# Optimization experiments

Measured on AMD Instinct MI355X. Metric: run time of the kernel, lower is better.

The kernel has to match this reference:

```python
import jax, jax.numpy as jnp
import numpy as np

B, T, C, H = 8, 2048, 1024, 128  # batch, seq, n_embed, head_size


def setup_inputs() -> dict:
    key = jax.random.key(0)
    ks = jax.random.split(key, 7)
    s = 1.0 / np.sqrt(C)
    return {
        "x": jax.random.normal(ks[0], (B, T, C), dtype=jnp.float32),
        "Wq": jax.random.uniform(ks[1], (C, H), jnp.float32, -s, s),
        "bq": jax.random.uniform(ks[2], (H,), jnp.float32, -s, s),
        "Wk": jax.random.uniform(ks[3], (C, H), jnp.float32, -s, s),
        "bk": jax.random.uniform(ks[4], (H,), jnp.float32, -s, s),
        "Wv": jax.random.uniform(ks[5], (C, H), jnp.float32, -s, s),
        "bv": jax.random.uniform(ks[6], (H,), jnp.float32, -s, s),
    }


def reference(x, Wq, bq, Wk, bk, Wv, bv):
    # Projections: [B, T, H]
    Q = jnp.einsum("btc,ch->bth", x, Wq) + bq
    K = jnp.einsum("btc,ch->bth", x, Wk) + bk
    V = jnp.einsum("btc,ch->bth", x, Wv) + bv
    # Scores scaled by n_embed**-0.5 (faithful to source, which uses C not head_size)
    scale = jnp.asarray(C, x.dtype) ** -0.5
    scores = jnp.einsum("bqh,bkh->bqk", Q, K) * scale  # [B, T, T]
    causal = jnp.tril(jnp.ones((T, T), dtype=bool))
    scores = jnp.where(causal, scores, jnp.asarray(-jnp.inf, x.dtype))
    attn = jax.nn.softmax(scores, axis=-1)
    # dropout p=0.0 (eval) -> identity
    return jnp.einsum("bqk,bkh->bqh", attn, V)
```

## Files before the change

kernel.cpp:

```cpp
#include <hip/hip_runtime.h>
#include <hip/hip_bf16.h>
#include <math.h>

typedef __attribute__((ext_vector_type(4))) float f32x4;
typedef __attribute__((ext_vector_type(8))) short s16x8;
typedef __attribute__((ext_vector_type(4))) short s16x4;

#define NB 8
#define NT 2048
#define NC 1024
#define NH 128
#define QSCALE 0.04508422002778f

__device__ __forceinline__ short f2bf(float f) {
  union { float f; unsigned u; } v; v.f = f;
  unsigned r = v.u + 0x7fffu + ((v.u >> 16) & 1u);
  return (short)(r >> 16);
}

__device__ __forceinline__ void glds16(const short* g, short* l) {
  __builtin_amdgcn_global_load_lds(
      (const __attribute__((address_space(1))) unsigned int*)g,
      (__attribute__((address_space(3))) unsigned int*)l, 16, 0, 0);
}

__global__ __launch_bounds__(256)
void wt_kernel(const float* __restrict__ Wq, const float* __restrict__ Wk,
               const float* __restrict__ Wv, short* __restrict__ Wt) {
  __shared__ short T[64 * 72];
  const int tid = threadIdx.x;
  const int k0 = blockIdx.x * 64, n0 = blockIdx.y * 64, proj = blockIdx.z;
  const float* W = (proj == 0) ? Wq : ((proj == 1) ? Wk : Wv);
#pragma unroll
  for (int u = 0; u < 4; u++) {
    int row = u * 16 + (tid >> 4);
    int col4 = (tid & 15) * 4;
    float4 v = *(const float4*)(W + (size_t)(k0 + row) * NH + n0 + col4);
    T[(col4 + 0) * 72 + row] = f2bf(v.x);
    T[(col4 + 1) * 72 + row] = f2bf(v.y);
    T[(col4 + 2) * 72 + row] = f2bf(v.z);
    T[(col4 + 3) * 72 + row] = f2bf(v.w);
  }
  __syncthreads();
#pragma unroll
  for (int u = 0; u < 2; u++) {
    int c = tid + 256 * u;
    int n = c >> 3, c8 = c & 7;
    s16x8 v = *(const s16x8*)(T + n * 72 + c8 * 8);
    *(s16x8*)(Wt + (size_t)proj * (NH * NC) + (size_t)(n0 + n) * NC + k0 + c8 * 8) = v;
  }
}

__global__ __launch_bounds__(256, 3)
void proj_kernel(const float* __restrict__ x, const short* __restrict__ Wt,
                 const float* __restrict__ bq, const float* __restrict__ bk,
                 const float* __restrict__ bv,
                 short* __restrict__ Qb, short* __restrict__ Kb, short* __restrict__ Vtb) {
  __shared__ __align__(16) short smem[2 * 12288];

  const int tid = threadIdx.x;
  const int w = tid >> 6, lane = tid & 63;
  const int lr = lane & 15, lg = lane >> 4;

  const int bid = blockIdx.x;
  const int orig = (bid & 7) * 96 + (bid >> 3);
  const int proj = orig >> 8;
  const int m0 = (orig & 255) * 64;

  const short* Wtp = Wt + (size_t)proj * (NH * NC);

  f32x4 acc[8];
#pragma unroll
  for (int i = 0; i < 8; i++) acc[i] = {0.f, 0.f, 0.f, 0.f};

  const int s0 = 2 * tid, s1 = 2 * tid + 1;
  const int ar0 = s0 >> 3, ac0 = s0 & 7, ar1 = s1 >> 3, ac1 = s1 & 7;
  const float* asrc0base = x + (size_t)(m0 + ar0) * NC + ((ac0 ^ (ar0 & 7)) * 8);
  const float* asrc1base = x + (size_t)(m0 + ar1) * NC + ((ac1 ^ (ar1 & 7)) * 8);

  float4 a00, a01, a10, a11;

  auto stageA_load = [&](int k0) {
    a00 = *(const float4*)(asrc0base + k0);
    a01 = *(const float4*)(asrc0base + k0 + 4);
    a10 = *(const float4*)(asrc1base + k0);
    a11 = *(const float4*)(asrc1base + k0 + 4);
  };
  auto stageA_write = [&](int buf) {
    s16x8 v;
    v[0] = f2bf(a00.x); v[1] = f2bf(a00.y); v[2] = f2bf(a00.z); v[3] = f2bf(a00.w);
    v[4] = f2bf(a01.x); v[5] = f2bf(a01.y); v[6] = f2bf(a01.z); v[7] = f2bf(a01.w);
    *(s16x8*)(smem + buf * 12288 + s0 * 8) = v;
    v[0] = f2bf(a10.x); v[1] = f2bf(a10.y); v[2] = f2bf(a10.z); v[3] = f2bf(a10.w);
    v[4] = f2bf(a11.x); v[5] = f2bf(a11.y); v[6] = f2bf(a11.z); v[7] = f2bf(a11.w);
    *(s16x8*)(smem + buf * 12288 + s1 * 8) = v;
  };
  auto stageB = [&](int buf, int k0) {
#pragma unroll
    for (int u = 0; u < 4; u++) {
      int g = w * 4 + u;
      int s = g * 64 + lane;
      int n = s >> 3, c8 = s & 7;
      const short* src = Wtp + (size_t)n * NC + k0 + ((c8 ^ (n & 7)) * 8);
      short* dst = smem + buf * 12288 + 4096 + g * 512;
      glds16(src, dst);
    }
  };

  stageA_load(0);
  stageB(0, 0);
  stageA_write(0);
  __syncthreads();

  for (int it = 0; it < 16; ++it) {
    int buf = it & 1, nb = buf ^ 1;
    if (it < 15) { stageA_load((it + 1) * 64); stageB(nb, (it + 1) * 64); }
    const short* A = smem + buf * 12288;
    const short* B = smem + buf * 12288 + 4096;
    const int arow = w * 16 + lr;
#pragma unroll
    for (int kc = 0; kc < 2; kc++) {
      s16x8 af = *(const s16x8*)(A + arow * 64 + (((kc * 4 + lg) ^ (arow & 7)) * 8));
#pragma unroll
      for (int ni = 0; ni < 8; ni++) {
        int brow = ni * 16 + lr;
        s16x8 bf = *(const s16x8*)(B + brow * 64 + (((kc * 4 + lg) ^ (brow & 7)) * 8));
        acc[ni] = __builtin_amdgcn_mfma_f32_16x16x32_bf16(af, bf, acc[ni], 0, 0, 0);
      }
    }
    if (it < 15) stageA_write(nb);
    __syncthreads();
  }

  const float* bias = (proj == 0) ? bq : ((proj == 1) ? bk : bv);
  const float scl = (proj == 0) ? QSCALE : 1.0f;
  short* Tr = smem;

  if (proj < 2) {
#pragma unroll
    for (int ni = 0; ni < 8; ni++) {
      float bn = bias[ni * 16 + lr];
#pragma unroll
      for (int r = 0; r < 4; r++) {
        int t = w * 16 + lg * 4 + r;
        Tr[t * 136 + ni * 16 + lr] = f2bf((acc[ni][r] + bn) * scl);
      }
    }
    __syncthreads();
    short* dst = (proj == 0) ? Qb : Kb;
#pragma unroll
    for (int i = 0; i < 4; i++) {
      int c = tid + 256 * i;
      int t = c >> 4, c8 = c & 15;
      s16x8 v = *(const s16x8*)(Tr + t * 136 + c8 * 8);
      *(s16x8*)(dst + (size_t)(m0 + t) * NH + c8 * 8) = v;
    }
  } else {
#pragma unroll
    for (int ni = 0; ni < 8; ni++) {
      float bn = bias[ni * 16 + lr];
      int d = ni * 16 + lr;
      int t = w * 16 + lg * 4;
      s16x4 v;
      v[0] = f2bf(acc[ni][0] + bn);
      v[1] = f2bf(acc[ni][1] + bn);
      v[2] = f2bf(acc[ni][2] + bn);
      v[3] = f2bf(acc[ni][3] + bn);
      *(s16x4*)(Tr + d * 72 + t) = v;
    }
    __syncthreads();
    int b = m0 >> 11, t0 = m0 & 2047;
#pragma unroll
    for (int i = 0; i < 4; i++) {
      int c = tid + 256 * i;
      int d = c >> 3, c8 = c & 7;
      s16x8 v = *(const s16x8*)(Tr + d * 72 + c8 * 8);
      *(s16x8*)(Vtb + (size_t)b * (NH * NT) + (size_t)d * NT + t0 + c8 * 8) = v;
    }
  }
}

__global__ __launch_bounds__(256, 3)
void attn_kernel(const short* __restrict__ Qb, const short* __restrict__ Kb,
                 const short* __restrict__ Vtb, float* __restrict__ out) {
  __shared__ float Cb[3][16][132];
  __shared__ float2 Ml[3][16];

  const int tid = threadIdx.x;
  const int w = tid >> 6, lane = tid & 63;
  const int lr = lane & 15, lg = lane >> 4;

  const int bid = blockIdx.x;
  const int orig = (bid & 7) * 64 + (bid >> 3);
  const int batch = orig >> 6;
  const int pairid = orig & 63;

  const short* Kp = Kb + (size_t)batch * NT * NH;
  const short* Vp = Vtb + (size_t)batch * NH * NT;

#pragma unroll 1
  for (int ph = 0; ph < 2; ph++) {
    const int j = ph ? (127 - pairid) : pairid;
    const int q0 = j * 16;
    const int q = q0 + lr;

    const short* Qrow = Qb + (size_t)(batch * NT + q) * NH;
    s16x8 qf[4];
#pragma unroll
    for (int dc = 0; dc < 4; dc++) qf[dc] = *(const s16x8*)(Qrow + dc * 32 + lg * 8);

    f32x4 acc[8];
#pragma unroll
    for (int i = 0; i < 8; i++) acc[i] = {0.f, 0.f, 0.f, 0.f};
    float m_run = -3.0e38f, l_run = 0.f;

    const int Nt = (q0 + 47) >> 5;

    for (int t = w; t < Nt; t += 4) {
      const int kv0 = t * 32;
      f32x4 st0 = {0.f, 0.f, 0.f, 0.f}, st1 = st0;
      const short* Kt = Kp + (size_t)(kv0 + lr) * NH + lg * 8;
#pragma unroll
      for (int dc = 0; dc < 4; dc++) {
        s16x8 k0f = *(const s16x8*)(Kt + dc * 32);
        s16x8 k1f = *(const s16x8*)(Kt + 16 * NH + dc * 32);
        st0 = __builtin_amdgcn_mfma_f32_16x16x32_bf16(k0f, qf[dc], st0, 0, 0, 0);
        st1 = __builtin_amdgcn_mfma_f32_16x16x32_bf16(k1f, qf[dc], st1, 0, 0, 0);
      }
      if (kv0 + 31 > q0) {
#pragma unroll
        for (int r = 0; r < 4; r++) {
          if (kv0 + lg * 4 + r > q) st0[r] = -3.0e38f;
          if (kv0 + 16 + lg * 4 + r > q) st1[r] = -3.0e38f;
        }
      }
      float tm = -3.0e38f;
#pragma unroll
      for (int r = 0; r < 4; r++) { tm = fmaxf(tm, st0[r]); tm = fmaxf(tm, st1[r]); }
      tm = fmaxf(tm, __shfl_xor(tm, 16, 64));
      tm = fmaxf(tm, __shfl_xor(tm, 32, 64));
      float m_new = fmaxf(m_run, tm);
      float corr = exp2f(m_run - m_new);
      float psum = 0.f;
      s16x8 pf;
#pragma unroll
      for (int r = 0; r < 4; r++) {
        float p0 = exp2f(st0[r] - m_new);
        float p1 = exp2f(st1[r] - m_new);
        psum += p0 + p1;
        pf[r] = f2bf(p0);
        pf[4 + r] = f2bf(p1);
      }
      psum += __shfl_xor(psum, 16, 64);
      psum += __shfl_xor(psum, 32, 64);
      l_run = l_run * corr + psum;
      m_run = m_new;
#pragma unroll
      for (int i = 0; i < 8; i++) acc[i] *= corr;
#pragma unroll
      for (int dm = 0; dm < 8; dm++) {
        const short* vp = Vp + (size_t)(dm * 16 + lr) * NT + kv0 + lg * 4;
        s16x4 v0 = *(const s16x4*)vp;
        s16x4 v1 = *(const s16x4*)(vp + 16);
        s16x8 vf = __builtin_shufflevector(v0, v1, 0, 1, 2, 3, 4, 5, 6, 7);
        acc[dm] = __builtin_amdgcn_mfma_f32_16x16x32_bf16(vf, pf, acc[dm], 0, 0, 0);
      }
    }

    __syncthreads();
    if (w > 0) {
#pragma unroll
      for (int dm = 0; dm < 8; dm++)
        *(f32x4*)&Cb[w - 1][lr][dm * 16 + lg * 4] = acc[dm];
      if (lg == 0) Ml[w - 1][lr] = make_float2(m_run, l_run);
    }
    __syncthreads();
    if (w == 0) {
      float2 ml0 = Ml[0][lr], ml1 = Ml[1][lr], ml2 = Ml[2][lr];
      float M = fmaxf(fmaxf(m_run, ml0.x), fmaxf(ml1.x, ml2.x));
      float c0 = exp2f(m_run - M);
      float c1 = exp2f(ml0.x - M);
      float c2 = exp2f(ml1.x - M);
      float c3 = exp2f(ml2.x - M);
      float lt = l_run * c0 + ml0.y * c1 + ml1.y * c2 + ml2.y * c3;
      float inv = 1.0f / lt;
      float* orow = out + (size_t)(batch * NT + q) * NH;
#pragma unroll
      for (int dm = 0; dm < 8; dm++) {
        f32x4 v = acc[dm] * c0;
        v += (*(const f32x4*)&Cb[0][lr][dm * 16 + lg * 4]) * c1;
        v += (*(const f32x4*)&Cb[1][lr][dm * 16 + lg * 4]) * c2;
        v += (*(const f32x4*)&Cb[2][lr][dm * 16 + lg * 4]) * c3;
        v *= inv;
        *(f32x4*)(orow + dm * 16 + lg * 4) = v;
      }
    }
    __syncthreads();
  }
}

extern "C" void kernel_launch(void* const* d_in, const int* in_sizes, int n_in,
                              void* d_out, int out_size, void* d_ws, size_t ws_size,
                              hipStream_t stream) {
  const float* x = (const float*)d_in[0];
  const float* Wq = (const float*)d_in[1];
  const float* bq = (const float*)d_in[2];
  const float* Wk = (const float*)d_in[3];
  const float* bk = (const float*)d_in[4];
  const float* Wv = (const float*)d_in[5];
  const float* bv = (const float*)d_in[6];
  float* out = (float*)d_out;

  char* ws = (char*)d_ws;
  short* Wt = (short*)ws;
  short* Qb = (short*)(ws + 786432);
  short* Kb = (short*)(ws + 786432 + 4194304);
  short* Vtb = (short*)(ws + 786432 + 2 * 4194304);

  wt_kernel<<<dim3(16, 2, 3), dim3(256), 0, stream>>>(Wq, Wk, Wv, Wt);
  proj_kernel<<<dim3(768), dim3(256), 0, stream>>>(x, Wt, bq, bk, bv, Qb, Kb, Vtb);
  attn_kernel<<<dim3(512), dim3(256), 0, stream>>>(Qb, Kb, Vtb, out);
}
```

Measured before the change: 221.4 us.

## Retile projection GEMM to 128x128 and split attention into KV-chunked partials with combine

The projection kernel now computes 128-row tiles across all 128 head columns. Each wave owns a 64x64 sub-tile, and x is prefetched through registers. Attention is restructured so each block handles 64 queries, with K and V staged into LDS via async global-to-LDS loads and double buffering. Long causal rows are split into 512-key chunks, and a separate combine kernel merges the partials. This aims to improve reuse and load balance, at the cost of an extra launch and fp32 partial traffic through the workspace.

```diff
diff --git a/kernel.cpp b/kernel.cpp
--- a/kernel.cpp
+++ b/kernel.cpp
@@ -11,6 +11,7 @@
 #define NC 1024
 #define NH 128
 #define QSCALE 0.04508422002778f
+#define PIECES 80
 
 __device__ __forceinline__ short f2bf(float f) {
   union { float f; unsigned u; } v; v.f = f;
@@ -51,86 +52,81 @@
   }
 }
 
-__global__ __launch_bounds__(256, 3)
+__global__ __launch_bounds__(256)
 void proj_kernel(const float* __restrict__ x, const short* __restrict__ Wt,
                  const float* __restrict__ bq, const float* __restrict__ bk,
                  const float* __restrict__ bv,
                  short* __restrict__ Qb, short* __restrict__ Kb, short* __restrict__ Vtb) {
-  __shared__ __align__(16) short smem[2 * 12288];
+  __shared__ __align__(16) short smem[17408];
+  short* As = smem;
+  short* Bs = smem + 8192;
 
   const int tid = threadIdx.x;
   const int w = tid >> 6, lane = tid & 63;
   const int lr = lane & 15, lg = lane >> 4;
-
-  const int bid = blockIdx.x;
-  const int orig = (bid & 7) * 96 + (bid >> 3);
-  const int proj = orig >> 8;
-  const int m0 = (orig & 255) * 64;
+  const int proj = blockIdx.x;
+  const int m0 = blockIdx.y * 128;
+  const int msub = (w & 1) * 64, nsub = (w >> 1) * 64;
 
   const short* Wtp = Wt + (size_t)proj * (NH * NC);
-
-  f32x4 acc[8];
-#pragma unroll
-  for (int i = 0; i < 8; i++) acc[i] = {0.f, 0.f, 0.f, 0.f};
-
-  const int s0 = 2 * tid, s1 = 2 * tid + 1;
-  const int ar0 = s0 >> 3, ac0 = s0 & 7, ar1 = s1 >> 3, ac1 = s1 & 7;
-  const float* asrc0base = x + (size_t)(m0 + ar0) * NC + ((ac0 ^ (ar0 & 7)) * 8);
-  const float* asrc1base = x + (size_t)(m0 + ar1) * NC + ((ac1 ^ (ar1 & 7)) * 8);
-
-  float4 a00, a01, a10, a11;
-
-  auto stageA_load = [&](int k0) {
-    a00 = *(const float4*)(asrc0base + k0);
-    a01 = *(const float4*)(asrc0base + k0 + 4);
-    a10 = *(const float4*)(asrc1base + k0);
-    a11 = *(const float4*)(asrc1base + k0 + 4);
+  const float* asrc = x + (size_t)(m0 + (tid >> 1)) * NC + (tid & 1) * 32;
+  const int arow = tid >> 1;
+
+  f32x4 acc[4][4];
+#pragma unroll
+  for (int i = 0; i < 4; i++)
+#pragma unroll
+    for (int j = 0; j < 4; j++) acc[i][j] = {0.f, 0.f, 0.f, 0.f};
+
+  float4 pa[8], pb_[8];
+#pragma unroll
+  for (int u = 0; u < 8; u++) pa[u] = *(const float4*)(asrc + u * 4);
+
+  auto body = [&](int s, float4 (&cur)[8], float4 (&nxt)[8]) {
+    const int k0 = s * 64;
+    if (s < 15) {
+#pragma unroll
+      for (int u = 0; u < 8; u++) nxt[u] = *(const float4*)(asrc + k0 + 64 + u * 4);
+    }
+#pragma unroll
+    for (int u = 0; u < 4; u++) {
+      float4 a = cur[2 * u], b2 = cur[2 * u + 1];
+      s16x8 v;
+      v[0] = f2bf(a.x); v[1] = f2bf(a.y); v[2] = f2bf(a.z); v[3] = f2bf(a.w);
+      v[4] = f2bf(b2.x); v[5] = f2bf(b2.y); v[6] = f2bf(b2.z); v[7] = f2bf(b2.w);
+      int cc = (tid & 1) * 4 + u;
+      *(s16x8*)(As + arow * 64 + ((cc ^ (arow & 7)) * 8)) = v;
+    }
+#pragma unroll
+    for (int u = 0; u < 4; u++) {
+      int boff = w * 4096 + u * 1024 + lane * 16;
+      int n = boff >> 7, cc = (boff >> 4) & 7;
+      glds16(Wtp + (size_t)n * NC + k0 + ((cc ^ (n & 7)) * 8), Bs + w * 2048 + u * 512);
+    }
+    __syncthreads();
+#pragma unroll
+    for (int kc = 0; kc < 2; kc++) {
+      s16x8 af[4], bf[4];
+#pragma unroll
+      for (int mi = 0; mi < 4; mi++) {
+        int row = msub + mi * 16 + lr;
+        af[mi] = *(const s16x8*)(As + row * 64 + (((kc * 4 + lg) ^ (lr & 7)) * 8));
+      }
+#pragma unroll
+      for (int ni = 0; ni < 4; ni++) {
+        int row = nsub + ni * 16 + lr;
+        bf[ni] = *(const s16x8*)(Bs + row * 64 + (((kc * 4 + lg) ^ (lr & 7)) * 8));
+      }
+#pragma unroll
+      for (int mi = 0; mi < 4; mi++)
+#pragma unroll
+        for (int ni = 0; ni < 4; ni++)
+          acc[mi][ni] = __builtin_amdgcn_mfma_f32_16x16x32_bf16(af[mi], bf[ni], acc[mi][ni], 0, 0, 0);
+    }
+    __syncthreads();
   };
-  auto stageA_write = [&](int buf) {
-    s16x8 v;
-    v[0] = f2bf(a00.x); v[1] = f2bf(a00.y); v[2] = f2bf(a00.z); v[3] = f2bf(a00.w);
-    v[4] = f2bf(a01.x); v[5] = f2bf(a01.y); v[6] = f2bf(a01.z); v[7] = f2bf(a01.w);
-    *(s16x8*)(smem + buf * 12288 + s0 * 8) = v;
-    v[0] = f2bf(a10.x); v[1] = f2bf(a10.y); v[2] = f2bf(a10.z); v[3] = f2bf(a10.w);
-    v[4] = f2bf(a11.x); v[5] = f2bf(a11.y); v[6] = f2bf(a11.z); v[7] = f2bf(a11.w);
-    *(s16x8*)(smem + buf * 12288 + s1 * 8) = v;
-  };
-  auto stageB = [&](int buf, int k0) {
-#pragma unroll
-    for (int u = 0; u < 4; u++) {
-      int g = w * 4 + u;
-      int s = g * 64 + lane;
-      int n = s >> 3, c8 = s & 7;
-      const short* src = Wtp + (size_t)n * NC + k0 + ((c8 ^ (n & 7)) * 8);
-      short* dst = smem + buf * 12288 + 4096 + g * 512;
-      glds16(src, dst);
-    }
-  };
-
-  stageA_load(0);
-  stageB(0, 0);
-  stageA_write(0);
-  __syncthreads();
-
-  for (int it = 0; it < 16; ++it) {
-    int buf = it & 1, nb = buf ^ 1;
-    if (it < 15) { stageA_load((it + 1) * 64); stageB(nb, (it + 1) * 64); }
-    const short* A = smem + buf * 12288;
-    const short* B = smem + buf * 12288 + 4096;
-    const int arow = w * 16 + lr;
-#pragma unroll
-    for (int kc = 0; kc < 2; kc++) {
-      s16x8 af = *(const s16x8*)(A + arow * 64 + (((kc * 4 + lg) ^ (arow & 7)) * 8));
-#pragma unroll
-      for (int ni = 0; ni < 8; ni++) {
-        int brow = ni * 16 + lr;
-        s16x8 bf = *(const s16x8*)(B + brow * 64 + (((kc * 4 + lg) ^ (brow & 7)) * 8));
-        acc[ni] = __builtin_amdgcn_mfma_f32_16x16x32_bf16(af, bf, acc[ni], 0, 0, 0);
-      }
-    }
-    if (it < 15) stageA_write(nb);
-    __syncthreads();
-  }
+
+  for (int ss = 0; ss < 8; ss++) { body(2 * ss, pa, pb_); body(2 * ss + 1, pb_, pa); }
 
   const float* bias = (proj == 0) ? bq : ((proj == 1) ? bk : bv);
   const float scl = (proj == 0) ? QSCALE : 1.0f;
@@ -138,165 +134,221 @@
 
   if (proj < 2) {
 #pragma unroll
-    for (int ni = 0; ni < 8; ni++) {
-      float bn = bias[ni * 16 + lr];
-#pragma unroll
-      for (int r = 0; r < 4; r++) {
-        int t = w * 16 + lg * 4 + r;
-        Tr[t * 136 + ni * 16 + lr] = f2bf((acc[ni][r] + bn) * scl);
-      }
-    }
+    for (int mi = 0; mi < 4; mi++)
+#pragma unroll
+      for (int ni = 0; ni < 4; ni++) {
+        float bn = bias[nsub + ni * 16 + lr];
+        int d = nsub + ni * 16 + lr;
+#pragma unroll
+        for (int r = 0; r < 4; r++) {
+          int t = msub + mi * 16 + lg * 4 + r;
+          Tr[t * 136 + d] = f2bf((acc[mi][ni][r] + bn) * scl);
+        }
+      }
     __syncthreads();
     short* dst = (proj == 0) ? Qb : Kb;
 #pragma unroll
-    for (int i = 0; i < 4; i++) {
+    for (int i = 0; i < 8; i++) {
       int c = tid + 256 * i;
-      int t = c >> 4, c8 = c & 15;
-      s16x8 v = *(const s16x8*)(Tr + t * 136 + c8 * 8);
-      *(s16x8*)(dst + (size_t)(m0 + t) * NH + c8 * 8) = v;
+      int t = c >> 4, cc = c & 15;
+      s16x8 v = *(const s16x8*)(Tr + t * 136 + cc * 8);
+      *(s16x8*)(dst + (size_t)(m0 + t) * NH + cc * 8) = v;
     }
   } else {
 #pragma unroll
-    for (int ni = 0; ni < 8; ni++) {
-      float bn = bias[ni * 16 + lr];
-      int d = ni * 16 + lr;
-      int t = w * 16 + lg * 4;
-      s16x4 v;
-      v[0] = f2bf(acc[ni][0] + bn);
-      v[1] = f2bf(acc[ni][1] + bn);
-      v[2] = f2bf(acc[ni][2] + bn);
-      v[3] = f2bf(acc[ni][3] + bn);
-      *(s16x4*)(Tr + d * 72 + t) = v;
-    }
-    __syncthreads();
-    int b = m0 >> 11, t0 = m0 & 2047;
-#pragma unroll
-    for (int i = 0; i < 4; i++) {
+    for (int mi = 0; mi < 4; mi++)
+#pragma unroll
+      for (int ni = 0; ni < 4; ni++) {
+        float bn = bias[nsub + ni * 16 + lr];
+        int d = nsub + ni * 16 + lr;
+        int t0 = msub + mi * 16 + lg * 4;
+        s16x4 v;
+        v[0] = f2bf(acc[mi][ni][0] + bn);
+        v[1] = f2bf(acc[mi][ni][1] + bn);
+        v[2] = f2bf(acc[mi][ni][2] + bn);
+        v[3] = f2bf(acc[mi][ni][3] + bn);
+        *(s16x4*)(Tr + d * 136 + t0) = v;
+      }
+    __syncthreads();
+    int b = m0 >> 11, t0g = m0 & 2047;
+#pragma unroll
+    for (int i = 0; i < 8; i++) {
       int c = tid + 256 * i;
-      int d = c >> 3, c8 = c & 7;
-      s16x8 v = *(const s16x8*)(Tr + d * 72 + c8 * 8);
-      *(s16x8*)(Vtb + (size_t)b * (NH * NT) + (size_t)d * NT + t0 + c8 * 8) = v;
-    }
-  }
-}
-
-__global__ __launch_bounds__(256, 3)
-void attn_kernel(const short* __restrict__ Qb, const short* __restrict__ Kb,
-                 const short* __restrict__ Vtb, float* __restrict__ out) {
-  __shared__ float Cb[3][16][132];
-  __shared__ float2 Ml[3][16];
+      int d = c >> 4, cc = c & 15;
+      s16x8 v = *(const s16x8*)(Tr + d * 136 + cc * 8);
+      *(s16x8*)(Vtb + (size_t)b * (NH * NT) + (size_t)d * NT + t0g + cc * 8) = v;
+    }
+  }
+}
+
+__global__ __launch_bounds__(256)
+void attn_partial(const short* __restrict__ Qb, const short* __restrict__ Kb,
+                  const short* __restrict__ Vtb, float* __restrict__ out,
+                  float* __restrict__ part, float* __restrict__ partml) {
+  __shared__ __align__(16) short smem[16384];
 
   const int tid = threadIdx.x;
   const int w = tid >> 6, lane = tid & 63;
   const int lr = lane & 15, lg = lane >> 4;
 
-  const int bid = blockIdx.x;
-  const int orig = (bid & 7) * 64 + (bid >> 3);
-  const int batch = orig >> 6;
-  const int pairid = orig & 63;
+  const int batch = blockIdx.x;
+  const int r = (PIECES - 1) - blockIdx.y;
+  int j = 0, pfx = 0;
+  while (pfx + (j >> 3) + 1 <= r) { pfx += (j >> 3) + 1; j++; }
+  const int c = r - pfx;
+  const int P = (j >> 3) + 1;
+  const int q0 = j * 64;
+  const int kv_begin = c * 512;
+  const int kv_end = min(kv_begin + 512, (j + 1) * 64);
+  const int nsteps = (kv_end - kv_begin) >> 5;
 
   const short* Kp = Kb + (size_t)batch * NT * NH;
   const short* Vp = Vtb + (size_t)batch * NH * NT;
-
-#pragma unroll 1
-  for (int ph = 0; ph < 2; ph++) {
-    const int j = ph ? (127 - pairid) : pairid;
-    const int q0 = j * 16;
-    const int q = q0 + lr;
-
-    const short* Qrow = Qb + (size_t)(batch * NT + q) * NH;
-    s16x8 qf[4];
-#pragma unroll
-    for (int dc = 0; dc < 4; dc++) qf[dc] = *(const s16x8*)(Qrow + dc * 32 + lg * 8);
-
-    f32x4 acc[8];
-#pragma unroll
-    for (int i = 0; i < 8; i++) acc[i] = {0.f, 0.f, 0.f, 0.f};
-    float m_run = -3.0e38f, l_run = 0.f;
-
-    const int Nt = (q0 + 47) >> 5;
-
-    for (int t = w; t < Nt; t += 4) {
-      const int kv0 = t * 32;
-      f32x4 st0 = {0.f, 0.f, 0.f, 0.f}, st1 = st0;
-      const short* Kt = Kp + (size_t)(kv0 + lr) * NH + lg * 8;
-#pragma unroll
-      for (int dc = 0; dc < 4; dc++) {
-        s16x8 k0f = *(const s16x8*)(Kt + dc * 32);
-        s16x8 k1f = *(const s16x8*)(Kt + 16 * NH + dc * 32);
-        st0 = __builtin_amdgcn_mfma_f32_16x16x32_bf16(k0f, qf[dc], st0, 0, 0, 0);
-        st1 = __builtin_amdgcn_mfma_f32_16x16x32_bf16(k1f, qf[dc], st1, 0, 0, 0);
-      }
-      if (kv0 + 31 > q0) {
-#pragma unroll
-        for (int r = 0; r < 4; r++) {
-          if (kv0 + lg * 4 + r > q) st0[r] = -3.0e38f;
-          if (kv0 + 16 + lg * 4 + r > q) st1[r] = -3.0e38f;
-        }
-      }
-      float tm = -3.0e38f;
-#pragma unroll
-      for (int r = 0; r < 4; r++) { tm = fmaxf(tm, st0[r]); tm = fmaxf(tm, st1[r]); }
-      tm = fmaxf(tm, __shfl_xor(tm, 16, 64));
-      tm = fmaxf(tm, __shfl_xor(tm, 32, 64));
-      float m_new = fmaxf(m_run, tm);
-      float corr = exp2f(m_run - m_new);
-      float psum = 0.f;
-      s16x8 pf;
-#pragma unroll
-      for (int r = 0; r < 4; r++) {
-        float p0 = exp2f(st0[r] - m_new);
-        float p1 = exp2f(st1[r] - m_new);
-        psum += p0 + p1;
-        pf[r] = f2bf(p0);
-        pf[4 + r] = f2bf(p1);
-      }
-      psum += __shfl_xor(psum, 16, 64);
-      psum += __shfl_xor(psum, 32, 64);
-      l_run = l_run * corr + psum;
-      m_run = m_new;
-#pragma unroll
-      for (int i = 0; i < 8; i++) acc[i] *= corr;
-#pragma unroll
-      for (int dm = 0; dm < 8; dm++) {
-        const short* vp = Vp + (size_t)(dm * 16 + lr) * NT + kv0 + lg * 4;
-        s16x4 v0 = *(const s16x4*)vp;
-        s16x4 v1 = *(const s16x4*)(vp + 16);
-        s16x8 vf = __builtin_shufflevector(v0, v1, 0, 1, 2, 3, 4, 5, 6, 7);
-        acc[dm] = __builtin_amdgcn_mfma_f32_16x16x32_bf16(vf, pf, acc[dm], 0, 0, 0);
-      }
-    }
-
-    __syncthreads();
-    if (w > 0) {
-#pragma unroll
-      for (int dm = 0; dm < 8; dm++)
-        *(f32x4*)&Cb[w - 1][lr][dm * 16 + lg * 4] = acc[dm];
-      if (lg == 0) Ml[w - 1][lr] = make_float2(m_run, l_run);
-    }
-    __syncthreads();
-    if (w == 0) {
-      float2 ml0 = Ml[0][lr], ml1 = Ml[1][lr], ml2 = Ml[2][lr];
-      float M = fmaxf(fmaxf(m_run, ml0.x), fmaxf(ml1.x, ml2.x));
-      float c0 = exp2f(m_run - M);
-      float c1 = exp2f(ml0.x - M);
-      float c2 = exp2f(ml1.x - M);
-      float c3 = exp2f(ml2.x - M);
-      float lt = l_run * c0 + ml0.y * c1 + ml1.y * c2 + ml2.y * c3;
-      float inv = 1.0f / lt;
-      float* orow = out + (size_t)(batch * NT + q) * NH;
-#pragma unroll
-      for (int dm = 0; dm < 8; dm++) {
-        f32x4 v = acc[dm] * c0;
-        v += (*(const f32x4*)&Cb[0][lr][dm * 16 + lg * 4]) * c1;
-        v += (*(const f32x4*)&Cb[1][lr][dm * 16 + lg * 4]) * c2;
-        v += (*(const f32x4*)&Cb[2][lr][dm * 16 + lg * 4]) * c3;
-        v *= inv;
-        *(f32x4*)(orow + dm * 16 + lg * 4) = v;
-      }
-    }
-    __syncthreads();
-  }
+  const int q = q0 + w * 16 + lr;
+
+  const short* Qrow = Qb + (size_t)(batch * NT + q) * NH;
+  s16x8 qf[4];
+#pragma unroll
+  for (int dc = 0; dc < 4; dc++) qf[dc] = *(const s16x8*)(Qrow + dc * 32 + lg * 8);
+
+  f32x4 acc[8];
+#pragma unroll
+  for (int i = 0; i < 8; i++) acc[i] = {0.f, 0.f, 0.f, 0.f};
+  float m_run = -3.0e38f, l_run = 0.f;
+
+  auto stage = [&](int buf, int kv0) {
+#pragma unroll
+    for (int u = 0; u < 2; u++) {
+      int boff = w * 2048 + u * 1024 + lane * 16;
+      int row = boff >> 8, ch = (boff >> 4) & 15;
+      int sch = (ch & 8) | ((ch & 7) ^ (row & 7));
+      glds16(Kp + (size_t)(kv0 + row) * NH + sch * 8, smem + buf * 4096 + w * 1024 + u * 512);
+    }
+#pragma unroll
+    for (int u = 0; u < 2; u++) {
+      int boff = w * 2048 + u * 1024 + lane * 16;
+      int d = boff >> 6, ch = (boff >> 4) & 3;
+      int sch = ch ^ (d & 3);
+      glds16(Vp + (size_t)d * NT + kv0 + sch * 8, smem + 8192 + buf * 4096 + w * 1024 + u * 512);
+    }
+  };
+
+  stage(0, kv_begin);
+  __syncthreads();
+
+  for (int s = 0; s < nsteps; s++) {
+    const int buf = s & 1;
+    const int kv0 = kv_begin + s * 32;
+    if (s + 1 < nsteps) stage(buf ^ 1, kv0 + 32);
+
+    const short* Kl = smem + buf * 4096;
+    const short* Vl = smem + 8192 + buf * 4096;
+
+    f32x4 st0 = {0.f, 0.f, 0.f, 0.f}, st1 = st0;
+#pragma unroll
+    for (int dc = 0; dc < 4; dc++) {
+      int ch = dc * 4 + lg;
+      int sch = (ch & 8) | ((ch & 7) ^ (lr & 7));
+      s16x8 k0f = *(const s16x8*)(Kl + lr * 128 + sch * 8);
+      s16x8 k1f = *(const s16x8*)(Kl + (16 + lr) * 128 + sch * 8);
+      st0 = __builtin_amdgcn_mfma_f32_16x16x32_bf16(k0f, qf[dc], st0, 0, 0, 0);
+      st1 = __builtin_amdgcn_mfma_f32_16x16x32_bf16(k1f, qf[dc], st1, 0, 0, 0);
+    }
+    if (kv0 + 31 > q0) {
+#pragma unroll
+      for (int rr = 0; rr < 4; rr++) {
+        if (kv0 + lg * 4 + rr > q) st0[rr] = -3.0e38f;
+        if (kv0 + 16 + lg * 4 + rr > q) st1[rr] = -3.0e38f;
+      }
+    }
+    float tm = -3.0e38f;
+#pragma unroll
+    for (int rr = 0; rr < 4; rr++) { tm = fmaxf(tm, st0[rr]); tm = fmaxf(tm, st1[rr]); }
+    tm = fmaxf(tm, __shfl_xor(tm, 16, 64));
+    tm = fmaxf(tm, __shfl_xor(tm, 32, 64));
+    float m_new = fmaxf(m_run, tm);
+    float corr = exp2f(m_run - m_new);
+    float psum = 0.f;
+    s16x8 pf;
+#pragma unroll
+    for (int rr = 0; rr < 4; rr++) {
+      float p0 = exp2f(st0[rr] - m_new);
+      float p1 = exp2f(st1[rr] - m_new);
+      psum += p0 + p1;
+      pf[rr] = f2bf(p0);
+      pf[4 + rr] = f2bf(p1);
+    }
+    psum += __shfl_xor(psum, 16, 64);
+    psum += __shfl_xor(psum, 32, 64);
+    l_run = l_run * corr + psum;
+    m_run = m_new;
+#pragma unroll
+    for (int i = 0; i < 8; i++) acc[i] *= corr;
+#pragma unroll
+    for (int dm = 0; dm < 8; dm++) {
+      int d = dm * 16 + lr;
+      const short* vb = Vl + d * 32;
+      int c0 = (lg >> 1) ^ (d & 3);
+      int c1 = c0 ^ 2;
+      s16x4 v0 = *(const s16x4*)(vb + c0 * 8 + (lg & 1) * 4);
+      s16x4 v1 = *(const s16x4*)(vb + c1 * 8 + (lg & 1) * 4);
+      s16x8 vf = __builtin_shufflevector(v0, v1, 0, 1, 2, 3, 4, 5, 6, 7);
+      acc[dm] = __builtin_amdgcn_mfma_f32_16x16x32_bf16(vf, pf, acc[dm], 0, 0, 0);
+    }
+    __syncthreads();
+  }
+
+  if (P == 1) {
+    const float inv = 1.f / l_run;
+    float* orow = out + (size_t)(batch * NT + q) * NH;
+#pragma unroll
+    for (int dm = 0; dm < 8; dm++) {
+      f32x4 v = acc[dm] * inv;
+      *(f32x4*)(orow + dm * 16 + lg * 4) = v;
+    }
+  } else {
+    float* pb = part + ((size_t)batch * PIECES + r) * 8192;
+    int ql = w * 16 + lr;
+#pragma unroll
+    for (int dm = 0; dm < 8; dm++)
+      *(f32x4*)(pb + ql * 128 + dm * 16 + lg * 4) = acc[dm];
+    if (lg == 0) {
+      float2* ml = (float2*)partml + ((size_t)batch * PIECES + r) * 64;
+      ml[ql] = make_float2(m_run, l_run);
+    }
+  }
+}
+
+__global__ __launch_bounds__(256)
+void attn_combine(const float* __restrict__ part, const float* __restrict__ partml,
+                  float* __restrict__ out) {
+  const int batch = blockIdx.x;
+  const int j = 8 + blockIdx.y;
+  int pfx = 0;
+  for (int jj = 0; jj < j; jj++) pfx += (jj >> 3) + 1;
+  const int P = (j >> 3) + 1;
+  const int tid = threadIdx.x;
+  const int ql = tid >> 2, d0 = (tid & 3) * 32;
+
+  const float2* mlb = (const float2*)partml + ((size_t)batch * PIECES + pfx) * 64 + ql;
+  float M = -3.0e38f;
+  for (int p = 0; p < P; p++) M = fmaxf(M, mlb[p * 64].x);
+  float L = 0.f;
+  f32x4 o[8];
+#pragma unroll
+  for (int u = 0; u < 8; u++) o[u] = {0.f, 0.f, 0.f, 0.f};
+  for (int p = 0; p < P; p++) {
+    float2 ml = mlb[p * 64];
+    float wgt = exp2f(ml.x - M);
+    L += wgt * ml.y;
+    const float* pb = part + ((size_t)batch * PIECES + pfx + p) * 8192 + ql * 128 + d0;
+#pragma unroll
+    for (int u = 0; u < 8; u++) o[u] += wgt * *(const f32x4*)(pb + u * 4);
+  }
+  const float inv = 1.f / L;
+  float* orow = out + ((size_t)batch * NT + j * 64 + ql) * NH + d0;
+#pragma unroll
+  for (int u = 0; u < 8; u++) *(f32x4*)(orow + u * 4) = o[u] * inv;
 }
 
 extern "C" void kernel_launch(void* const* d_in, const int* in_sizes, int n_in,
@@ -316,8 +368,11 @@
   short* Qb = (short*)(ws + 786432);
   short* Kb = (short*)(ws + 786432 + 4194304);
   short* Vtb = (short*)(ws + 786432 + 2 * 4194304);
+  float* part = (float*)(ws + 13369344);
+  float* partml = (float*)(ws + 13369344 + 20971520);
 
   wt_kernel<<<dim3(16, 2, 3), dim3(256), 0, stream>>>(Wq, Wk, Wv, Wt);
-  proj_kernel<<<dim3(768), dim3(256), 0, stream>>>(x, Wt, bq, bk, bv, Qb, Kb, Vtb);
-  attn_kernel<<<dim3(512), dim3(256), 0, stream>>>(Qb, Kb, Vtb, out);
-}
+  proj_kernel<<<dim3(3, 128), dim3(256), 0, stream>>>(x, Wt, bq, bk, bv, Qb, Kb, Vtb);
+  attn_partial<<<dim3(8, PIECES), dim3(256), 0, stream>>>(Qb, Kb, Vtb, out, part, partml);
+  attn_combine<<<dim3(8, 24), dim3(256), 0, stream>>>(part, partml, out);
+}
```

After: 206.6 us. 1.07x faster.
